# Optimization experiments

Measured on AMD Instinct MI355X. Metric: run time of the kernel, lower is better.

Reference implementation:

```python
import jax, jax.numpy as jnp
import numpy as np

B, T, D, N = 32, 2048, 512, 512


def setup_inputs() -> dict:
    key = jax.random.key(0)
    ks = jax.random.split(key, 16)
    s_in = 1.0 / np.sqrt(D)
    s_h = 1.0 / np.sqrt(N)
    inp = {
        "x": jax.random.normal(ks[0], (B, T, D), dtype=jnp.float32),
        "W_i": jax.random.normal(ks[1], (D, N), dtype=jnp.float32) * s_in,
        "U_i": jax.random.normal(ks[2], (N, N), dtype=jnp.float32) * s_h,
        "W_f": jax.random.normal(ks[3], (D, N), dtype=jnp.float32) * s_in,
        "U_f": jax.random.normal(ks[4], (N, N), dtype=jnp.float32) * s_h,
        "W_g": jax.random.normal(ks[5], (D, N), dtype=jnp.float32) * s_in,
        "U_g": jax.random.normal(ks[6], (N, N), dtype=jnp.float32) * s_h,
        "W_c": jax.random.normal(ks[7], (D, N), dtype=jnp.float32) * s_in,
        "U_c": jax.random.normal(ks[8], (N, N), dtype=jnp.float32) * s_h,
        "W_o": jax.random.normal(ks[9], (N, N), dtype=jnp.float32) * s_h,
        "b_i": jnp.zeros((N,), dtype=jnp.float32),
        "b_f": jnp.zeros((N,), dtype=jnp.float32),
        "b_g": jnp.zeros((N,), dtype=jnp.float32),
        "b_c": jnp.zeros((N,), dtype=jnp.float32),
        "b_o": jnp.zeros((N,), dtype=jnp.float32),
    }
    return inp


def _lstm_forward(x, W_i, U_i, W_f, U_f, W_g, U_g, W_c, U_c, W_o,
                  b_i, b_f, b_g, b_c, b_o):
    # Precompute input-to-gate projections for all timesteps (same math,
    # hoisted out of the recurrence): [T, B, N] each
    xt = jnp.swapaxes(x, 0, 1)  # [T, B, N? no, D] -> [T, B, D]
    xi = jnp.einsum('tbd,dn->tbn', xt, W_i) + b_i
    xf = jnp.einsum('tbd,dn->tbn', xt, W_f) + b_f
    xg = jnp.einsum('tbd,dn->tbn', xt, W_g) + b_g
    xc = jnp.einsum('tbd,dn->tbn', xt, W_c) + b_c

    h0 = jnp.zeros((x.shape[0], U_i.shape[0]), dtype=x.dtype)
    c0 = jnp.zeros_like(h0)

    def step(carry, gates_t):
        h, c = carry
        xi_t, xf_t, xg_t, xc_t = gates_t
        i = jax.nn.sigmoid(xi_t + h @ U_i)
        f = jax.nn.sigmoid(xf_t + h @ U_f)
        g = jax.nn.sigmoid(xg_t + h @ U_g)  # original applies nonlin_i to g
        c_tilda = jnp.tanh(xc_t + h @ U_c)
        c_new = f * c + i * c_tilda
        h_new = g * jnp.tanh(c_new)
        return (h_new, c_new), h_new

    _, hs = jax.lax.scan(step, (h0, c0), (xi, xf, xg, xc))  # hs: [T, B, N]
    # output_fn: relu(h @ W_o + b_o), applied per timestep
    out = jax.nn.relu(jnp.einsum('tbn,nm->tbm', hs, W_o) + b_o)
    return jnp.swapaxes(out, 0, 1)  # [B, T, N]


def reference(x, W_i, U_i, W_f, U_f, W_g, U_g, W_c, U_c, W_o,
              b_i, b_f, b_g, b_c, b_o):
    return _lstm_forward(x, W_i, U_i, W_f, U_f, W_g, U_g, W_c, U_c, W_o,
                         b_i, b_f, b_g, b_c, b_o)
```

## Files before the change

kernel.cpp:

```cpp
#include <hip/hip_runtime.h>
#include <stdint.h>

#define B_ 32
#define T_ 2048
#define D_ 512
#define N_ 512
#define NG 2048

typedef _Float16 f16;
typedef _Float16 half2v __attribute__((ext_vector_type(2)));
typedef _Float16 half8  __attribute__((ext_vector_type(8)));
typedef float    float4v __attribute__((ext_vector_type(4)));
typedef unsigned long long u64;

union U32H2 { unsigned u; half2v h; };
union U4H8  { uint4 u; half8 h; };

__global__ void prep_cast(const float* __restrict__ x, f16* __restrict__ x16) {
    long i = ((long)blockIdx.x * 256 + threadIdx.x) * 4;
    float4 v = *(const float4*)(x + i);
    union { f16 h[4]; uint2 u; } pk;
    pk.h[0] = (f16)v.x; pk.h[1] = (f16)v.y; pk.h[2] = (f16)v.z; pk.h[3] = (f16)v.w;
    *(uint2*)(x16 + i) = pk.u;
}

__global__ void prep_w(const float* __restrict__ Wi, const float* __restrict__ Ui,
                       const float* __restrict__ Wf, const float* __restrict__ Uf,
                       const float* __restrict__ Wg, const float* __restrict__ Ug,
                       const float* __restrict__ Wc, const float* __restrict__ Uc,
                       const float* __restrict__ Wo,
                       const float* __restrict__ bi, const float* __restrict__ bff,
                       const float* __restrict__ bg, const float* __restrict__ bc,
                       f16* __restrict__ wt, f16* __restrict__ ut,
                       f16* __restrict__ wot, float* __restrict__ bias)
{
    const int y = blockIdx.y;
    const int e = blockIdx.x * 256 + threadIdx.x;
    if (y < 4) {
        const float* src = (y == 0) ? Wi : (y == 1) ? Wf : (y == 2) ? Wg : Wc;
        int col = e >> 9, d = e & 511;
        wt[(long)y * 512 * 512 + e] = (f16)src[(long)d * 512 + col];
    } else if (y < 8) {
        const float* src = (y == 4) ? Ui : (y == 5) ? Uf : (y == 6) ? Ug : Uc;
        int col = e >> 9, d = e & 511;
        ut[(long)(y - 4) * 512 * 512 + e] = (f16)src[(long)d * 512 + col];
    } else if (y == 8) {
        int col = e >> 9, d = e & 511;
        wot[e] = (f16)Wo[(long)d * 512 + col];
    } else {
        if (e < 2048) {
            const float* bsrc = (e < 512) ? bi : (e < 1024) ? bff : (e < 1536) ? bg : bc;
            bias[e] = bsrc[e & 511];
        }
    }
}

__launch_bounds__(256)
__global__ void gemm_xw(const f16* __restrict__ A, const f16* __restrict__ Bt,
                        const float* __restrict__ bias, f16* __restrict__ C)
{
    __shared__ f16 sA[128 * 32];
    __shared__ f16 sB[128 * 32];
    const int tid = threadIdx.x;
    const int m0 = blockIdx.y * 128;
    const int n0 = blockIdx.x * 128;
    const int wave = tid >> 6, lane = tid & 63;
    const int wm = wave >> 1, wn = wave & 1;
    const int lrow = lane & 15, quad = lane >> 4;

    float4v acc[4][4];
#pragma unroll
    for (int i = 0; i < 4; i++)
#pragma unroll
        for (int j = 0; j < 4; j++) acc[i][j] = (float4v){0.f, 0.f, 0.f, 0.f};

    const int srow = tid >> 2;
    const int sk8 = (tid & 3) * 8;

    for (int k0 = 0; k0 < 512; k0 += 32) {
#pragma unroll
        for (int rr = 0; rr < 128; rr += 64) {
            const int row = rr + srow;
            *(uint4*)&sA[row * 32 + sk8] = *(const uint4*)&A[(long)(m0 + row) * 512 + k0 + sk8];
            *(uint4*)&sB[row * 32 + sk8] = *(const uint4*)&Bt[(long)(n0 + row) * 512 + k0 + sk8];
        }
        __syncthreads();
        half8 af[4], bf[4];
#pragma unroll
        for (int mi = 0; mi < 4; mi++)
            af[mi] = *(half8*)&sA[(wm * 64 + mi * 16 + lrow) * 32 + quad * 8];
#pragma unroll
        for (int ni = 0; ni < 4; ni++)
            bf[ni] = *(half8*)&sB[(wn * 64 + ni * 16 + lrow) * 32 + quad * 8];
#pragma unroll
        for (int mi = 0; mi < 4; mi++)
#pragma unroll
            for (int ni = 0; ni < 4; ni++)
                acc[mi][ni] = __builtin_amdgcn_mfma_f32_16x16x32_f16(af[mi], bf[ni], acc[mi][ni], 0, 0, 0);
        __syncthreads();
    }
#pragma unroll
    for (int mi = 0; mi < 4; mi++)
#pragma unroll
        for (int ni = 0; ni < 4; ni++)
#pragma unroll
            for (int r = 0; r < 4; r++) {
                int m = m0 + wm * 64 + mi * 16 + quad * 4 + r;
                int n = n0 + wn * 64 + ni * 16 + lrow;
                C[(long)m * NG + n] = (f16)(acc[mi][ni][r] + bias[n]);
            }
}

__launch_bounds__(256)
__global__ void gemm_hw(const f16* __restrict__ A, const f16* __restrict__ Bt,
                        const float* __restrict__ bias, float* __restrict__ out)
{
    __shared__ f16 sA[128 * 32];
    __shared__ f16 sB[128 * 32];
    const int tid = threadIdx.x;
    const int m0 = blockIdx.y * 128;
    const int n0 = blockIdx.x * 128;
    const int wave = tid >> 6, lane = tid & 63;
    const int wm = wave >> 1, wn = wave & 1;
    const int lrow = lane & 15, quad = lane >> 4;

    float4v acc[4][4];
#pragma unroll
    for (int i = 0; i < 4; i++)
#pragma unroll
        for (int j = 0; j < 4; j++) acc[i][j] = (float4v){0.f, 0.f, 0.f, 0.f};

    const int srow = tid >> 2;
    const int sk8 = (tid & 3) * 8;

    for (int k0 = 0; k0 < 512; k0 += 32) {
#pragma unroll
        for (int rr = 0; rr < 128; rr += 64) {
            const int row = rr + srow;
            *(uint4*)&sA[row * 32 + sk8] = *(const uint4*)&A[(long)(m0 + row) * 512 + k0 + sk8];
            *(uint4*)&sB[row * 32 + sk8] = *(const uint4*)&Bt[(long)(n0 + row) * 512 + k0 + sk8];
        }
        __syncthreads();
        half8 af[4], bf[4];
#pragma unroll
        for (int mi = 0; mi < 4; mi++)
            af[mi] = *(half8*)&sA[(wm * 64 + mi * 16 + lrow) * 32 + quad * 8];
#pragma unroll
        for (int ni = 0; ni < 4; ni++)
            bf[ni] = *(half8*)&sB[(wn * 64 + ni * 16 + lrow) * 32 + quad * 8];
#pragma unroll
        for (int mi = 0; mi < 4; mi++)
#pragma unroll
            for (int ni = 0; ni < 4; ni++)
                acc[mi][ni] = __builtin_amdgcn_mfma_f32_16x16x32_f16(af[mi], bf[ni], acc[mi][ni], 0, 0, 0);
        __syncthreads();
    }
#pragma unroll
    for (int mi = 0; mi < 4; mi++)
#pragma unroll
        for (int ni = 0; ni < 4; ni++)
#pragma unroll
            for (int r = 0; r < 4; r++) {
                int m = m0 + wm * 64 + mi * 16 + quad * 4 + r;
                int n = n0 + wn * 64 + ni * 16 + lrow;
                float v = acc[mi][ni][r] + bias[n];
                v = fmaxf(v, 0.f);
                int t = m >> 5, b = m & 31;
                out[(long)b * (T_ * (long)N_) + (long)t * N_ + n] = v;
            }
}

__launch_bounds__(512, 2)
__global__ void lstm_rec(const f16* __restrict__ Ut,
                         const f16* __restrict__ xpre,
                         u64* __restrict__ hg64,
                         unsigned* __restrict__ hs32,
                         int unused)
{
    const int tid = threadIdx.x;
    const int bb = blockIdx.x & 31;
    const int s  = blockIdx.x >> 5;
    const int w    = tid >> 6;
    const int lane = tid & 63;
    const int quad = lane >> 4;
    const int lcol = lane & 15;
    const int g0    = w >> 1;
    const int ebase = (w & 1) * 32;

    __shared__ __align__(16) unsigned hbuf32[256];
    __shared__ float prelds[256];

    half8 bf0[16], bf1[16];
    {
        const int e0 = ebase + lcol;
        const int e1 = ebase + 16 + lcol;
        const f16* bp0 = Ut + (long)(g0 * 512 + s * 64 + e0) * 512 + quad * 8;
        const f16* bp1 = Ut + (long)(g0 * 512 + s * 64 + e1) * 512 + quad * 8;
#pragma unroll
        for (int ks = 0; ks < 16; ks++) {
            bf0[ks] = *(const half8*)(bp0 + ks * 32);
            bf1[ks] = *(const half8*)(bp1 + ks * 32);
        }
    }

    if (tid < 256) hbuf32[tid] = 0u;
    float c0 = 0.f, c1 = 0.f;
    __syncthreads();

    const unsigned* xq = (const unsigned*)(xpre + (long)bb * T_ * NG + s * 64) + tid;

    for (int t = 0; t < T_; ++t) {
        unsigned xpp0 = 0, xpp1 = 0, xpp2 = 0, xpp3 = 0;
        if (tid < 32) {
            const long o = (long)t * 1024;
            xpp0 = xq[o];
            xpp1 = xq[o + 256];
            xpp2 = xq[o + 512];
            xpp3 = xq[o + 768];
        }

        if (t > 0 && tid < 256) {
            const u64* slot = hg64 + (size_t)(t & 1) * 8192 + bb * 256 + tid;
            const unsigned tag = (unsigned)t;
            u64 v;
            while ((unsigned)((v = __hip_atomic_load(slot, __ATOMIC_RELAXED,
                                                     __HIP_MEMORY_SCOPE_AGENT)) >> 32) != tag)
                __builtin_amdgcn_s_sleep(1);
            hbuf32[tid] = (unsigned)v;
        }
        __syncthreads();

        float4v a0 = {0.f, 0.f, 0.f, 0.f}, a1 = {0.f, 0.f, 0.f, 0.f};
        float4v a2 = {0.f, 0.f, 0.f, 0.f}, a3 = {0.f, 0.f, 0.f, 0.f};
#pragma unroll
        for (int ks = 0; ks < 16; ks += 2) {
            U4H8 av0, av1;
            av0.u = *(const uint4*)&hbuf32[ks * 16 + quad * 4];
            av1.u = *(const uint4*)&hbuf32[(ks + 1) * 16 + quad * 4];
            a0 = __builtin_amdgcn_mfma_f32_16x16x32_f16(av0.h, bf0[ks],     a0, 0, 0, 0);
            a1 = __builtin_amdgcn_mfma_f32_16x16x32_f16(av0.h, bf1[ks],     a1, 0, 0, 0);
            a2 = __builtin_amdgcn_mfma_f32_16x16x32_f16(av1.h, bf0[ks + 1], a2, 0, 0, 0);
            a3 = __builtin_amdgcn_mfma_f32_16x16x32_f16(av1.h, bf1[ks + 1], a3, 0, 0, 0);
        }
        if (lane < 32)
            prelds[w * 32 + lane] = (lane < 16) ? (a0[0] + a2[0]) : (a1[0] + a3[0]);
        __syncthreads();

        if (tid < 32) {
            const int c2 = 2 * tid;
            U32H2 xi_, xf_, xg_, xc_;
            xi_.u = xpp0; xf_.u = xpp1; xg_.u = xpp2; xc_.u = xpp3;
            float pi0 = prelds[c2]       + (float)xi_.h[0], pi1 = prelds[c2 + 1]       + (float)xi_.h[1];
            float pf0 = prelds[64 + c2]  + (float)xf_.h[0], pf1 = prelds[64 + c2 + 1]  + (float)xf_.h[1];
            float pg0 = prelds[128 + c2] + (float)xg_.h[0], pg1 = prelds[128 + c2 + 1] + (float)xg_.h[1];
            float pc0 = prelds[192 + c2] + (float)xc_.h[0], pc1 = prelds[192 + c2 + 1] + (float)xc_.h[1];
            float gi0 = 1.f / (1.f + __expf(-pi0)), gi1 = 1.f / (1.f + __expf(-pi1));
            float gf0 = 1.f / (1.f + __expf(-pf0)), gf1 = 1.f / (1.f + __expf(-pf1));
            float gg0 = 1.f / (1.f + __expf(-pg0)), gg1 = 1.f / (1.f + __expf(-pg1));
            float ct0 = tanhf(pc0), ct1 = tanhf(pc1);
            c0 = gf0 * c0 + gi0 * ct0;
            c1 = gf1 * c1 + gi1 * ct1;
            float h0 = gg0 * tanhf(c0);
            float h1 = gg1 * tanhf(c1);
            union { f16 h[2]; unsigned u; } pk;
            pk.h[0] = (f16)h0; pk.h[1] = (f16)h1;
            u64 pv = ((u64)(unsigned)(t + 1) << 32) | (u64)pk.u;
            __hip_atomic_store(hg64 + (size_t)((t + 1) & 1) * 8192 + bb * 256 + s * 32 + tid,
                               pv, __ATOMIC_RELAXED, __HIP_MEMORY_SCOPE_AGENT);
            hs32[((long)t * B_ + bb) * 256 + s * 32 + tid] = pk.u;
        }
    }
}

extern "C" void kernel_launch(void* const* d_in, const int* in_sizes, int n_in,
                              void* d_out, int out_size, void* d_ws, size_t ws_size,
                              hipStream_t stream)
{
    const float* x  = (const float*)d_in[0];
    const float* Wi = (const float*)d_in[1];
    const float* Ui = (const float*)d_in[2];
    const float* Wf = (const float*)d_in[3];
    const float* Uf = (const float*)d_in[4];
    const float* Wg = (const float*)d_in[5];
    const float* Ug = (const float*)d_in[6];
    const float* Wc = (const float*)d_in[7];
    const float* Uc = (const float*)d_in[8];
    const float* Wo = (const float*)d_in[9];
    const float* bi = (const float*)d_in[10];
    const float* bf = (const float*)d_in[11];
    const float* bg = (const float*)d_in[12];
    const float* bc = (const float*)d_in[13];
    const float* bo = (const float*)d_in[14];

    char* ws = (char*)d_ws;
    f16*      x16   = (f16*)(ws + 0L);
    f16*      xpre  = (f16*)(ws + 67108864L);
    f16*      hs    = (f16*)(ws + 335544320L);
    f16*      wt    = (f16*)(ws + 402653184L);
    f16*      ut    = (f16*)(ws + 404750336L);
    f16*      wot   = (f16*)(ws + 406847488L);
    float*    bias  = (float*)(ws + 407371776L);
    u64*      hg64  = (u64*)(ws + 407379968L);

    prep_cast<<<dim3(32768), dim3(256), 0, stream>>>(x, x16);
    prep_w<<<dim3(1024, 10), dim3(256), 0, stream>>>(Wi, Ui, Wf, Uf, Wg, Ug, Wc, Uc, Wo,
                                                     bi, bf, bg, bc, wt, ut, wot, bias);
    gemm_xw<<<dim3(16, 512), dim3(256), 0, stream>>>(x16, wt, bias, xpre);
    lstm_rec<<<dim3(256), dim3(512), 0, stream>>>(ut, xpre, hg64, (unsigned*)hs, 0);
    gemm_hw<<<dim3(4, 512), dim3(256), 0, stream>>>(hs, wot, bo, (float*)d_out);
}
```

Before: 4.442 ms.

## Prefetch next-step input projections, spread gate math over 64 lanes, fast activations

```diff
diff --git a/kernel.cpp b/kernel.cpp
--- a/kernel.cpp
+++ b/kernel.cpp
@@ -15,6 +15,14 @@
 
 union U32H2 { unsigned u; half2v h; };
 union U4H8  { uint4 u; half8 h; };
+union H16U  { f16 h; unsigned short s; };
+
+static __device__ __forceinline__ float fast_sigmoid(float x) {
+    return __builtin_amdgcn_rcpf(1.f + __expf(-x));
+}
+static __device__ __forceinline__ float fast_tanh(float x) {
+    return 1.f - 2.f * __builtin_amdgcn_rcpf(1.f + __expf(2.f * x));
+}
 
 __global__ void prep_cast(const float* __restrict__ x, f16* __restrict__ x16) {
     long i = ((long)blockIdx.x * 256 + threadIdx.x) * 4;
@@ -204,21 +212,17 @@
     }
 
     if (tid < 256) hbuf32[tid] = 0u;
-    float c0 = 0.f, c1 = 0.f;
+    float cst = 0.f;
     __syncthreads();
 
-    const unsigned* xq = (const unsigned*)(xpre + (long)bb * T_ * NG + s * 64) + tid;
+    const f16* xb = xpre + (long)bb * T_ * NG + s * 64 + tid;
+
+    f16 xc_i = (f16)0, xc_f = (f16)0, xc_g = (f16)0, xc_c = (f16)0;
+    if (tid < 64) {
+        xc_i = xb[0]; xc_f = xb[512]; xc_g = xb[1024]; xc_c = xb[1536];
+    }
 
     for (int t = 0; t < T_; ++t) {
-        unsigned xpp0 = 0, xpp1 = 0, xpp2 = 0, xpp3 = 0;
-        if (tid < 32) {
-            const long o = (long)t * 1024;
-            xpp0 = xq[o];
-            xpp1 = xq[o + 256];
-            xpp2 = xq[o + 512];
-            xpp3 = xq[o + 768];
-        }
-
         if (t > 0 && tid < 256) {
             const u64* slot = hg64 + (size_t)(t & 1) * 8192 + bb * 256 + tid;
             const unsigned tag = (unsigned)t;
@@ -230,6 +234,12 @@
         }
         __syncthreads();
 
+        f16 xn_i = (f16)0, xn_f = (f16)0, xn_g = (f16)0, xn_c = (f16)0;
+        if (t < T_ - 1 && tid < 64) {
+            const f16* p = xb + (long)(t + 1) * NG;
+            xn_i = p[0]; xn_f = p[512]; xn_g = p[1024]; xn_c = p[1536];
+        }
+
         float4v a0 = {0.f, 0.f, 0.f, 0.f}, a1 = {0.f, 0.f, 0.f, 0.f};
         float4v a2 = {0.f, 0.f, 0.f, 0.f}, a3 = {0.f, 0.f, 0.f, 0.f};
 #pragma unroll
@@ -246,29 +256,31 @@
             prelds[w * 32 + lane] = (lane < 16) ? (a0[0] + a2[0]) : (a1[0] + a3[0]);
         __syncthreads();
 
-        if (tid < 32) {
-            const int c2 = 2 * tid;
-            U32H2 xi_, xf_, xg_, xc_;
-            xi_.u = xpp0; xf_.u = xpp1; xg_.u = xpp2; xc_.u = xpp3;
-            float pi0 = prelds[c2]       + (float)xi_.h[0], pi1 = prelds[c2 + 1]       + (float)xi_.h[1];
-            float pf0 = prelds[64 + c2]  + (float)xf_.h[0], pf1 = prelds[64 + c2 + 1]  + (float)xf_.h[1];
-            float pg0 = prelds[128 + c2] + (float)xg_.h[0], pg1 = prelds[128 + c2 + 1] + (float)xg_.h[1];
-            float pc0 = prelds[192 + c2] + (float)xc_.h[0], pc1 = prelds[192 + c2 + 1] + (float)xc_.h[1];
-            float gi0 = 1.f / (1.f + __expf(-pi0)), gi1 = 1.f / (1.f + __expf(-pi1));
-            float gf0 = 1.f / (1.f + __expf(-pf0)), gf1 = 1.f / (1.f + __expf(-pf1));
-            float gg0 = 1.f / (1.f + __expf(-pg0)), gg1 = 1.f / (1.f + __expf(-pg1));
-            float ct0 = tanhf(pc0), ct1 = tanhf(pc1);
-            c0 = gf0 * c0 + gi0 * ct0;
-            c1 = gf1 * c1 + gi1 * ct1;
-            float h0 = gg0 * tanhf(c0);
-            float h1 = gg1 * tanhf(c1);
-            union { f16 h[2]; unsigned u; } pk;
-            pk.h[0] = (f16)h0; pk.h[1] = (f16)h1;
-            u64 pv = ((u64)(unsigned)(t + 1) << 32) | (u64)pk.u;
-            __hip_atomic_store(hg64 + (size_t)((t + 1) & 1) * 8192 + bb * 256 + s * 32 + tid,
-                               pv, __ATOMIC_RELAXED, __HIP_MEMORY_SCOPE_AGENT);
-            hs32[((long)t * B_ + bb) * 256 + s * 32 + tid] = pk.u;
-        }
+        if (tid < 64) {
+            float pre_i = prelds[tid]       + (float)xc_i;
+            float pre_f = prelds[64 + tid]  + (float)xc_f;
+            float pre_g = prelds[128 + tid] + (float)xc_g;
+            float pre_c = prelds[192 + tid] + (float)xc_c;
+            float gi = fast_sigmoid(pre_i);
+            float gf = fast_sigmoid(pre_f);
+            float gg = fast_sigmoid(pre_g);
+            float ct = fast_tanh(pre_c);
+            cst = gf * cst + gi * ct;
+            float h = gg * fast_tanh(cst);
+
+            H16U cv; cv.h = (f16)h;
+            unsigned hx = (unsigned)cv.s;
+            unsigned lo = __shfl(hx, 2 * lane);
+            unsigned hi = __shfl(hx, 2 * lane + 1);
+            if (lane < 32) {
+                unsigned pk = lo | (hi << 16);
+                u64 pv = ((u64)(unsigned)(t + 1) << 32) | (u64)pk;
+                __hip_atomic_store(hg64 + (size_t)((t + 1) & 1) * 8192 + bb * 256 + s * 32 + lane,
+                                   pv, __ATOMIC_RELAXED, __HIP_MEMORY_SCOPE_AGENT);
+                hs32[((long)t * B_ + bb) * 256 + s * 32 + lane] = pk;
+            }
+        }
+        xc_i = xn_i; xc_f = xn_f; xc_g = xn_g; xc_c = xn_c;
     }
 }
 
```

Result: faster. 3.699 ms (-16.7%).
